# Kernel tuning notes

Hardware: AMD Instinct MI355X
Metric: run time of the kernel (lower is better)

The kernel has to match this reference:

```python
import jax, jax.numpy as jnp
import numpy as np

B = 4
S = 1024          # per-sequence length (equal for all sequences)
HQ = 32           # query heads
HK = 8            # kv heads (GQA)
D = 128           # head dim


def setup_inputs() -> dict:
    key = jax.random.key(0)
    k1, k2, k3 = jax.random.split(key, 3)
    total = B * S
    q = jax.random.normal(k1, (total, HQ, D), dtype=jnp.float32)
    k = jax.random.normal(k2, (total, HK, D), dtype=jnp.float32)
    v = jax.random.normal(k3, (total, HK, D), dtype=jnp.float32)
    cu = (jnp.arange(B + 1, dtype=jnp.int32) * S)
    return {
        "q": q, "k": k, "v": v,
        "cu_seqlens_q": cu, "cu_seqlens_k": cu,
        "max_seqlen_q": S, "max_seqlen_k": S,
    }


def reference(q, k, v, cu_seqlens_q, cu_seqlens_k, max_seqlen_q, max_seqlen_k):
    # Varlen causal GQA attention (prefill path of Attention.forward).
    # All sequences have equal length S = max_seqlen_q, so the packed varlen
    # layout is exactly a reshape to (B, S, H, D) -- same math as the
    # per-sequence Python loop in attention_varlen_func.
    total, Hq, Dh = q.shape
    Hk = k.shape[1]
    g = Hq // Hk                      # GQA group size
    Sq = int(max_seqlen_q)
    Bn = total // Sq
    scale = 1.0 / (Dh ** 0.5)

    qb = q.reshape(Bn, Sq, Hk, g, Dh)  # (B,S,Hk,g,D)
    kb = k.reshape(Bn, Sq, Hk, Dh)     # (B,S,Hk,D)
    vb = v.reshape(Bn, Sq, Hk, Dh)

    scores = jnp.einsum('bqhgd,bkhd->bhgqk', qb, kb) * scale  # (B,Hk,g,S,S)
    causal_mask = jnp.triu(jnp.ones((Sq, Sq), dtype=bool), k=1)
    scores = jnp.where(causal_mask, -jnp.inf, scores)
    attn = jax.nn.softmax(scores, axis=-1)
    out = jnp.einsum('bhgqk,bkhd->bqhgd', attn, vb)           # (B,S,Hk,g,D)
    return out.reshape(total, Hq, Dh)
```

## Files before the change

### kernel.cpp

```cpp
#include <hip/hip_runtime.h>
#include <hip/hip_bf16.h>
#include <stdint.h>


typedef __bf16 v8bf __attribute__((ext_vector_type(8)));
typedef __bf16 v4bf __attribute__((ext_vector_type(4)));
typedef float  v16f __attribute__((ext_vector_type(16)));

#define NB  4
#define NS  1024
#define NHQ 32
#define NHK 8
#define ND  128
#define BQ  128
#define BK  64
#define VOFF (8u << 20)

#define KOFF(r) (16*((r)>>3) + ((((r)>>2)&1)*4) + ((r)&3))

__global__ __launch_bounds__(256)
void prep(const float* __restrict__ kg, const float* __restrict__ vg,
          char* __restrict__ ws)
{
  const int tid = threadIdx.x;
  const int blk = blockIdx.x;
  if (blk < 4096) {
    int gid = blk * 256 + tid;
    int i  = gid & 31;
    int s  = (gid >> 5) & (NS - 1);
    int hk = (gid >> 15) & 7;
    int b  = gid >> 18;
    float4 f = *(const float4*)(kg + ((size_t)((b * NS + s) * NHK + hk)) * ND + 4 * i);
    v4bf kb;
    kb[0]=(__bf16)f.x; kb[1]=(__bf16)f.y; kb[2]=(__bf16)f.z; kb[3]=(__bf16)f.w;
    int t  = s >> 6;
    int c  = (s >> 5) & 1;
    int kk = s & 31;
    int mu = (kk & 3) + 4 * ((kk >> 3) & 1)
           + 8 * (2 * ((kk >> 4) & 1) + ((kk >> 2) & 1));
    int fidx  = c * 8 + (i >> 2);
    int halfb = (i >> 1) & 1;
    int byte  = fidx * 1024 + halfb * 512 + mu * 16 + ((4 * i) & 7) * 2;
    size_t tb = (size_t)((b * 8 + hk) * 16 + t) << 14;
    *(v4bf*)(ws + tb + byte) = kb;
  } else {
    int vid = (blk - 4096) * 256 + tid;
    int d  = vid & 127;
    int g  = (vid >> 7) & 7;
    int t  = (vid >> 10) & 15;
    int hk = (vid >> 14) & 7;
    int b  = vid >> 17;
    const float* vp = vg + ((size_t)((b * NS + t * 64 + g * 8) * NHK + hk)) * ND + d;
    v8bf w;
    #pragma unroll
    for (int e = 0; e < 8; ++e) w[e] = (__bf16)vp[(size_t)e * (NHK * ND)];
    int byte = (d * 8 + (g ^ ((d >> 1) & 7))) * 16;
    size_t tb = (size_t)((b * 8 + hk) * 16 + t) << 14;
    *(v8bf*)(ws + VOFF + tb + byte) = w;
  }
}

__global__ __launch_bounds__(256, 2)
void fattn(const float* __restrict__ qg, const char* __restrict__ kvg,
           float* __restrict__ og)
{
  __shared__ __align__(16) char  Vt[2][16384];
  __shared__ __align__(16) float alq[4 * 32];

  const int tid  = threadIdx.x;
  const int lane = tid & 63;
  const int wave = tid >> 6;
  const int half = lane >> 5;
  const int l31  = lane & 31;

  const int bx = blockIdx.x;
  const int hk = bx & 7;
  const int t6 = bx >> 3;
  const int b  = t6 >> 4;
  const int m6 = t6 & 15;
  const int p  = m6 >> 2;
  const int h  = hk * 4 + (m6 & 3);

  const float scale = 0.12751879523604785f;
  const int kvtile = (b * 8 + hk) * 16;

  auto dmaV = [&](int t_, char* dst) {
    const char* src = kvg + VOFF + ((size_t)(kvtile + t_) << 14);
    #pragma unroll
    for (int i = 0; i < 4; ++i) {
      int c = wave * 4 + i;
      __builtin_amdgcn_global_load_lds(
        (const __attribute__((address_space(1))) void*)(src + c * 1024 + lane * 16),
        (__attribute__((address_space(3))) void*)(dst + c * 1024),
        16, 0, 0);
    }
  };

  dmaV(0, Vt[0]);
  int cur = 0;

  for (int ph = 0; ph < 2; ++ph) {
    const int qt = ph ? (7 - p) : p;
    const int wv = ph ? (3 - wave) : wave;
    const int q0 = qt * BQ;
    const int wqb = q0 + wv * 32;
    const int qglob = wqb + l31;
    const int ntiles = 2 * (qt + 1);

    v8bf qf[8];
    {
      const float* qp = qg + ((size_t)((b * NS + qglob) * NHQ + h)) * ND + half * 8;
      #pragma unroll
      for (int dM = 0; dM < 8; ++dM) {
        float4 f0 = *(const float4*)(qp + dM * 16);
        float4 f1 = *(const float4*)(qp + dM * 16 + 4);
        v8bf t;
        t[0]=(__bf16)(f0.x*scale); t[1]=(__bf16)(f0.y*scale);
        t[2]=(__bf16)(f0.z*scale); t[3]=(__bf16)(f0.w*scale);
        t[4]=(__bf16)(f1.x*scale); t[5]=(__bf16)(f1.y*scale);
        t[6]=(__bf16)(f1.z*scale); t[7]=(__bf16)(f1.w*scale);
        qf[dM] = t;
      }
    }

    v16f accO[4];
    #pragma unroll
    for (int dt = 0; dt < 4; ++dt)
      #pragma unroll
      for (int e = 0; e < 16; ++e) accO[dt][e] = 0.f;
    float m_run = -INFINITY, l_run = 0.f;

    for (int t = 0; t < ntiles; ++t) {
      const int k0 = t * BK;

      asm volatile("s_waitcnt vmcnt(0)" ::: "memory");
      __syncthreads();

      if (t + 1 < ntiles)      dmaV(t + 1, Vt[cur ^ 1]);
      else if (ph == 0)        dmaV(0, Vt[cur ^ 1]);

      if (k0 <= wqb + 31) {
        const v8bf* kf = (const v8bf*)(kvg + ((size_t)(kvtile + t) << 14) + lane * 16);
        v8bf ka0[8], ka1[8];
        #pragma unroll
        for (int f = 0; f < 8; ++f) ka0[f] = kf[(size_t)f * 64];
        #pragma unroll
        for (int f = 0; f < 8; ++f) ka1[f] = kf[(size_t)(f + 8) * 64];

        v16f s0, s1;
        #pragma unroll
        for (int e = 0; e < 16; ++e) { s0[e] = 0.f; s1[e] = 0.f; }
        __builtin_amdgcn_s_setprio(1);
        #pragma unroll
        for (int dM = 0; dM < 8; ++dM)
          s0 = __builtin_amdgcn_mfma_f32_32x32x16_bf16(ka0[dM], qf[dM], s0, 0, 0, 0);
        #pragma unroll
        for (int dM = 0; dM < 8; ++dM)
          s1 = __builtin_amdgcn_mfma_f32_32x32x16_bf16(ka1[dM], qf[dM], s1, 0, 0, 0);
        __builtin_amdgcn_s_setprio(0);
        if (k0 + BK > wqb) {
          #pragma unroll
          for (int r = 0; r < 16; ++r) {
            int key = k0 + KOFF(r) + half * 8;
            if (key > qglob)      s0[r] = -INFINITY;
            if (key + 32 > qglob) s1[r] = -INFINITY;
          }
        }
        float m0 = s0[0];
        #pragma unroll
        for (int r = 1; r < 16; ++r) m0 = fmaxf(m0, s0[r]);
        #pragma unroll
        for (int r = 0; r < 16; ++r) m0 = fmaxf(m0, s1[r]);
        m0 = fmaxf(m0, __shfl_xor(m0, 32));
        float mn = fmaxf(m_run, m0);
        float rs = 0.f;
        #pragma unroll
        for (int r = 0; r < 16; ++r) { float pp = exp2f(s0[r] - mn); s0[r] = pp; rs += pp; }
        #pragma unroll
        for (int r = 0; r < 16; ++r) { float pp = exp2f(s1[r] - mn); s1[r] = pp; rs += pp; }
        rs += __shfl_xor(rs, 32);
        if (__any(m0 > m_run)) {
          float al = exp2f(m_run - mn);
          if (half == 0) alq[wave * 32 + l31] = al;
          float4 alf[4];
          #pragma unroll
          for (int c = 0; c < 4; ++c)
            alf[c] = *(const float4*)(&alq[wave * 32 + 8 * c + 4 * half]);
          #pragma unroll
          for (int dt = 0; dt < 4; ++dt)
            #pragma unroll
            for (int r = 0; r < 16; ++r)
              accO[dt][r] *= ((const float*)&alf[r >> 2])[r & 3];
          l_run = l_run * al + rs;
        } else {
          l_run += rs;
        }
        m_run = mn;
        const char* vtr = Vt[cur];
        __builtin_amdgcn_s_setprio(1);
        #pragma unroll
        for (int C = 0; C < 2; ++C) {
          #pragma unroll
          for (int cp = 0; cp < 2; ++cp) {
            v8bf pf;
            #pragma unroll
            for (int e = 0; e < 8; ++e)
              pf[e] = (__bf16)(C == 0 ? s0[cp * 8 + e] : s1[cp * 8 + e]);
            int g = (C * 2 + cp) * 2 + half;
            #pragma unroll
            for (int dt = 0; dt < 4; ++dt) {
              int d = dt * 32 + l31;
              v8bf vb = *(const v8bf*)(vtr + (d * 8 + (g ^ ((l31 >> 1) & 7))) * 16);
              accO[dt] = __builtin_amdgcn_mfma_f32_32x32x16_bf16(pf, vb, accO[dt], 0, 0, 0);
            }
          }
        }
        __builtin_amdgcn_s_setprio(0);
      }
      cur ^= 1;
    }

    if (half == 0) alq[wave * 32 + l31] = 1.f / l_run;
    float4 invf[4];
    #pragma unroll
    for (int c = 0; c < 4; ++c)
      invf[c] = *(const float4*)(&alq[wave * 32 + 8 * c + 4 * half]);
    #pragma unroll
    for (int dt = 0; dt < 4; ++dt) {
      #pragma unroll
      for (int r = 0; r < 16; ++r) {
        int qrow = (r & 3) + 8 * (r >> 2) + 4 * half;
        float* op = og + ((size_t)((b * NS + wqb + qrow) * NHQ + h)) * ND;
        op[dt * 32 + l31] = accO[dt][r] * ((const float*)&invf[r >> 2])[r & 3];
      }
    }
  }
}

extern "C" void kernel_launch(void* const* d_in, const int* in_sizes, int n_in,
                              void* d_out, int out_size, void* d_ws, size_t ws_size,
                              hipStream_t stream) {
  const float* q = (const float*)d_in[0];
  const float* k = (const float*)d_in[1];
  const float* v = (const float*)d_in[2];
  float* out = (float*)d_out;
  char* ws = (char*)d_ws;
  prep<<<dim3(4096 + 2048), 256, 0, stream>>>(k, v, ws);
  fattn<<<dim3(NB * NHQ * 4), 256, 0, stream>>>(q, ws, out);
}
```

Before: 200.3 us.

## Split KV range across two wave groups with LDS-staged K/V and merge

Doubles the block to 512 threads so two groups of four waves each process alternate 32-key tiles, then merges their softmax states and partial outputs through shared memory. K and V for a tile are interleaved in one 16KB workspace block and DMA'd together into LDS, replacing the per-wave global K loads. The exp is switched to a raw v_exp_f32, and the max and sum reductions become trees. This aims for more waves in flight and better latency hiding, but it adds an epilogue merge with three extra barriers and smaller per-wave tiles.

New measurement: 297.0 us. +48.3%, slower.

```diff
diff --git a/kernel.cpp b/kernel.cpp
--- a/kernel.cpp
+++ b/kernel.cpp
@@ -13,10 +13,13 @@
 #define NHK 8
 #define ND  128
 #define BQ  128
-#define BK  64
-#define VOFF (8u << 20)
+#define BK  32
 
 #define KOFF(r) (16*((r)>>3) + ((((r)>>2)&1)*4) + ((r)&3))
+
+__device__ __forceinline__ float fexp2(float x) {
+  float r; asm("v_exp_f32 %0, %1" : "=v"(r) : "v"(x)); return r;
+}
 
 __global__ __launch_bounds__(256)
 void prep(const float* __restrict__ kg, const float* __restrict__ vg,
@@ -33,45 +36,48 @@
     float4 f = *(const float4*)(kg + ((size_t)((b * NS + s) * NHK + hk)) * ND + 4 * i);
     v4bf kb;
     kb[0]=(__bf16)f.x; kb[1]=(__bf16)f.y; kb[2]=(__bf16)f.z; kb[3]=(__bf16)f.w;
-    int t  = s >> 6;
-    int c  = (s >> 5) & 1;
+    int t  = s >> 5;
     int kk = s & 31;
     int mu = (kk & 3) + 4 * ((kk >> 3) & 1)
            + 8 * (2 * ((kk >> 4) & 1) + ((kk >> 2) & 1));
-    int fidx  = c * 8 + (i >> 2);
+    int dM    = i >> 2;
     int halfb = (i >> 1) & 1;
-    int byte  = fidx * 1024 + halfb * 512 + mu * 16 + ((4 * i) & 7) * 2;
-    size_t tb = (size_t)((b * 8 + hk) * 16 + t) << 14;
+    int byte  = dM * 1024 + halfb * 512 + mu * 16 + ((4 * i) & 7) * 2;
+    size_t tb = (size_t)((b * 8 + hk) * 32 + t) << 14;
     *(v4bf*)(ws + tb + byte) = kb;
   } else {
     int vid = (blk - 4096) * 256 + tid;
     int d  = vid & 127;
-    int g  = (vid >> 7) & 7;
-    int t  = (vid >> 10) & 15;
+    int g  = (vid >> 7) & 3;
+    int t  = (vid >> 9) & 31;
     int hk = (vid >> 14) & 7;
     int b  = vid >> 17;
-    const float* vp = vg + ((size_t)((b * NS + t * 64 + g * 8) * NHK + hk)) * ND + d;
+    const float* vp = vg + ((size_t)((b * NS + t * 32 + g * 8) * NHK + hk)) * ND + d;
     v8bf w;
     #pragma unroll
     for (int e = 0; e < 8; ++e) w[e] = (__bf16)vp[(size_t)e * (NHK * ND)];
-    int byte = (d * 8 + (g ^ ((d >> 1) & 7))) * 16;
-    size_t tb = (size_t)((b * 8 + hk) * 16 + t) << 14;
-    *(v8bf*)(ws + VOFF + tb + byte) = w;
+    int byte = (d >> 1) * 128 + ((g ^ ((d >> 1) & 3)) * 32) + (d & 1) * 16;
+    size_t tb = (size_t)((b * 8 + hk) * 32 + t) << 14;
+    *(v8bf*)(ws + tb + 8192 + byte) = w;
   }
 }
 
-__global__ __launch_bounds__(256, 2)
+__global__ __launch_bounds__(512, 4)
 void fattn(const float* __restrict__ qg, const char* __restrict__ kvg,
            float* __restrict__ og)
 {
-  __shared__ __align__(16) char  Vt[2][16384];
-  __shared__ __align__(16) float alq[4 * 32];
+  __shared__ __align__(16) char  KV[2][32768];
+  __shared__ __align__(16) float alq[8 * 32];
+  __shared__ __align__(16) float mex[2 * 4 * 32];
+  __shared__ __align__(16) float lex[2 * 4 * 32];
 
   const int tid  = threadIdx.x;
   const int lane = tid & 63;
   const int wave = tid >> 6;
   const int half = lane >> 5;
   const int l31  = lane & 31;
+  const int rs4  = wave & 3;
+  const int kh   = wave >> 2;
 
   const int bx = blockIdx.x;
   const int hk = bx & 7;
@@ -82,10 +88,10 @@
   const int h  = hk * 4 + (m6 & 3);
 
   const float scale = 0.12751879523604785f;
-  const int kvtile = (b * 8 + hk) * 16;
-
-  auto dmaV = [&](int t_, char* dst) {
-    const char* src = kvg + VOFF + ((size_t)(kvtile + t_) << 14);
+  const int kvtile = (b * 8 + hk) * 32;
+
+  auto dma = [&](int s_, char* dst) {
+    const char* src = kvg + ((size_t)(kvtile + 2 * s_) << 14);
     #pragma unroll
     for (int i = 0; i < 4; ++i) {
       int c = wave * 4 + i;
@@ -96,16 +102,16 @@
     }
   };
 
-  dmaV(0, Vt[0]);
-  int cur = 0;
-
   for (int ph = 0; ph < 2; ++ph) {
     const int qt = ph ? (7 - p) : p;
-    const int wv = ph ? (3 - wave) : wave;
+    const int rv = ph ? (3 - rs4) : rs4;
     const int q0 = qt * BQ;
-    const int wqb = q0 + wv * 32;
+    const int wqb = q0 + rv * 32;
     const int qglob = wqb + l31;
-    const int ntiles = 2 * (qt + 1);
+    const int nsteps = 2 * (qt + 1);
+
+    dma(0, KV[0]);
+    int cur = 0;
 
     v8bf qf[8];
     {
@@ -130,57 +136,48 @@
       for (int e = 0; e < 16; ++e) accO[dt][e] = 0.f;
     float m_run = -INFINITY, l_run = 0.f;
 
-    for (int t = 0; t < ntiles; ++t) {
-      const int k0 = t * BK;
-
+    for (int s = 0; s < nsteps; ++s) {
       asm volatile("s_waitcnt vmcnt(0)" ::: "memory");
       __syncthreads();
-
-      if (t + 1 < ntiles)      dmaV(t + 1, Vt[cur ^ 1]);
-      else if (ph == 0)        dmaV(0, Vt[cur ^ 1]);
-
-      if (k0 <= wqb + 31) {
-        const v8bf* kf = (const v8bf*)(kvg + ((size_t)(kvtile + t) << 14) + lane * 16);
-        v8bf ka0[8], ka1[8];
-        #pragma unroll
-        for (int f = 0; f < 8; ++f) ka0[f] = kf[(size_t)f * 64];
-        #pragma unroll
-        for (int f = 0; f < 8; ++f) ka1[f] = kf[(size_t)(f + 8) * 64];
-
-        v16f s0, s1;
-        #pragma unroll
-        for (int e = 0; e < 16; ++e) { s0[e] = 0.f; s1[e] = 0.f; }
+      if (s + 1 < nsteps) dma(s + 1, KV[cur ^ 1]);
+
+      const int k0w = (2 * s + kh) * 32;
+      if (k0w <= wqb + 31) {
+        const char* kb = KV[cur] + kh * 16384;
+        v16f s0;
+        #pragma unroll
+        for (int e = 0; e < 16; ++e) s0[e] = 0.f;
         __builtin_amdgcn_s_setprio(1);
         #pragma unroll
-        for (int dM = 0; dM < 8; ++dM)
-          s0 = __builtin_amdgcn_mfma_f32_32x32x16_bf16(ka0[dM], qf[dM], s0, 0, 0, 0);
-        #pragma unroll
-        for (int dM = 0; dM < 8; ++dM)
-          s1 = __builtin_amdgcn_mfma_f32_32x32x16_bf16(ka1[dM], qf[dM], s1, 0, 0, 0);
+        for (int dM = 0; dM < 8; ++dM) {
+          v8bf ka = *(const v8bf*)(kb + dM * 1024 + lane * 16);
+          s0 = __builtin_amdgcn_mfma_f32_32x32x16_bf16(ka, qf[dM], s0, 0, 0, 0);
+        }
         __builtin_amdgcn_s_setprio(0);
-        if (k0 + BK > wqb) {
-          #pragma unroll
-          for (int r = 0; r < 16; ++r) {
-            int key = k0 + KOFF(r) + half * 8;
-            if (key > qglob)      s0[r] = -INFINITY;
-            if (key + 32 > qglob) s1[r] = -INFINITY;
-          }
-        }
-        float m0 = s0[0];
-        #pragma unroll
-        for (int r = 1; r < 16; ++r) m0 = fmaxf(m0, s0[r]);
-        #pragma unroll
-        for (int r = 0; r < 16; ++r) m0 = fmaxf(m0, s1[r]);
+        if (k0w + BK > wqb) {
+          #pragma unroll
+          for (int r = 0; r < 16; ++r)
+            if (k0w + KOFF(r) + half * 8 > qglob) s0[r] = -INFINITY;
+        }
+        float t8[8];
+        #pragma unroll
+        for (int i = 0; i < 8; ++i) t8[i] = fmaxf(s0[i], s0[i + 8]);
+        #pragma unroll
+        for (int i = 0; i < 4; ++i) t8[i] = fmaxf(t8[i], t8[i + 4]);
+        float m0 = fmaxf(fmaxf(t8[0], t8[2]), fmaxf(t8[1], t8[3]));
         m0 = fmaxf(m0, __shfl_xor(m0, 32));
         float mn = fmaxf(m_run, m0);
-        float rs = 0.f;
-        #pragma unroll
-        for (int r = 0; r < 16; ++r) { float pp = exp2f(s0[r] - mn); s0[r] = pp; rs += pp; }
-        #pragma unroll
-        for (int r = 0; r < 16; ++r) { float pp = exp2f(s1[r] - mn); s1[r] = pp; rs += pp; }
+        #pragma unroll
+        for (int r = 0; r < 16; ++r) s0[r] = fexp2(s0[r] - mn);
+        float u8[8];
+        #pragma unroll
+        for (int i = 0; i < 8; ++i) u8[i] = s0[i] + s0[i + 8];
+        #pragma unroll
+        for (int i = 0; i < 4; ++i) u8[i] = u8[i] + u8[i + 4];
+        float rs = (u8[0] + u8[2]) + (u8[1] + u8[3]);
         rs += __shfl_xor(rs, 32);
         if (__any(m0 > m_run)) {
-          float al = exp2f(m_run - mn);
+          float al = fexp2(m_run - mn);
           if (half == 0) alq[wave * 32 + l31] = al;
           float4 alf[4];
           #pragma unroll
@@ -196,23 +193,19 @@
           l_run += rs;
         }
         m_run = mn;
-        const char* vtr = Vt[cur];
         __builtin_amdgcn_s_setprio(1);
         #pragma unroll
-        for (int C = 0; C < 2; ++C) {
-          #pragma unroll
-          for (int cp = 0; cp < 2; ++cp) {
-            v8bf pf;
-            #pragma unroll
-            for (int e = 0; e < 8; ++e)
-              pf[e] = (__bf16)(C == 0 ? s0[cp * 8 + e] : s1[cp * 8 + e]);
-            int g = (C * 2 + cp) * 2 + half;
-            #pragma unroll
-            for (int dt = 0; dt < 4; ++dt) {
-              int d = dt * 32 + l31;
-              v8bf vb = *(const v8bf*)(vtr + (d * 8 + (g ^ ((l31 >> 1) & 7))) * 16);
-              accO[dt] = __builtin_amdgcn_mfma_f32_32x32x16_bf16(pf, vb, accO[dt], 0, 0, 0);
-            }
+        for (int cp = 0; cp < 2; ++cp) {
+          v8bf pf;
+          #pragma unroll
+          for (int e = 0; e < 8; ++e) pf[e] = (__bf16)s0[cp * 8 + e];
+          int g = cp * 2 + half;
+          #pragma unroll
+          for (int dt = 0; dt < 4; ++dt) {
+            int dh = dt * 16 + (l31 >> 1);
+            v8bf vb = *(const v8bf*)(kb + 8192 + dh * 128
+                        + ((g ^ (dh & 3)) * 32) + (l31 & 1) * 16);
+            accO[dt] = __builtin_amdgcn_mfma_f32_32x32x16_bf16(pf, vb, accO[dt], 0, 0, 0);
           }
         }
         __builtin_amdgcn_s_setprio(0);
@@ -220,18 +213,70 @@
       cur ^= 1;
     }
 
-    if (half == 0) alq[wave * 32 + l31] = 1.f / l_run;
-    float4 invf[4];
-    #pragma unroll
-    for (int c = 0; c < 4; ++c)
-      invf[c] = *(const float4*)(&alq[wave * 32 + 8 * c + 4 * half]);
-    #pragma unroll
-    for (int dt = 0; dt < 4; ++dt) {
-      #pragma unroll
-      for (int r = 0; r < 16; ++r) {
-        int qrow = (r & 3) + 8 * (r >> 2) + 4 * half;
-        float* op = og + ((size_t)((b * NS + wqb + qrow) * NHQ + h)) * ND;
-        op[dt * 32 + l31] = accO[dt][r] * ((const float*)&invf[r >> 2])[r & 3];
+    if (half == 0) mex[(kh * 4 + rs4) * 32 + l31] = m_run;
+    __syncthreads();
+    float m_oth = mex[((kh ^ 1) * 4 + rs4) * 32 + l31];
+    float M = fmaxf(m_run, m_oth);
+    float a = fexp2(m_run - M);
+    float lw = l_run * a;
+    if (half == 0) { alq[wave * 32 + l31] = a; lex[(kh * 4 + rs4) * 32 + l31] = lw; }
+    {
+      float4 af[4];
+      #pragma unroll
+      for (int c = 0; c < 4; ++c)
+        af[c] = *(const float4*)(&alq[wave * 32 + 8 * c + 4 * half]);
+      #pragma unroll
+      for (int dt = 0; dt < 4; ++dt)
+        #pragma unroll
+        for (int r = 0; r < 16; ++r)
+          accO[dt][r] *= ((const float*)&af[r >> 2])[r & 3];
+    }
+    float* mscr = (float*)&KV[0][0];
+    if (kh == 1) {
+      #pragma unroll
+      for (int dt = 0; dt < 4; ++dt) {
+        int col = dt * 32 + l31;
+        #pragma unroll
+        for (int q = 0; q < 4; ++q) {
+          int qi = 2 * q + half;
+          float4 w = make_float4(accO[dt][4*q], accO[dt][4*q+1],
+                                 accO[dt][4*q+2], accO[dt][4*q+3]);
+          *(float4*)(mscr + rs4 * 4096 + col * 32 + ((qi ^ (col & 7)) << 2)) = w;
+        }
+      }
+    }
+    __syncthreads();
+    float l_fin = 1.f;
+    if (kh == 0) {
+      l_fin = lw + lex[(4 + rs4) * 32 + l31];
+      #pragma unroll
+      for (int dt = 0; dt < 4; ++dt) {
+        int col = dt * 32 + l31;
+        #pragma unroll
+        for (int q = 0; q < 4; ++q) {
+          int qi = 2 * q + half;
+          float4 r4 = *(const float4*)(mscr + rs4 * 4096 + col * 32 + ((qi ^ (col & 7)) << 2));
+          accO[dt][4*q]   += r4.x; accO[dt][4*q+1] += r4.y;
+          accO[dt][4*q+2] += r4.z; accO[dt][4*q+3] += r4.w;
+        }
+      }
+    }
+    __syncthreads();
+
+    if (kh == 0) {
+      if (half == 0) alq[wave * 32 + l31] = 1.f / l_fin;
+      float4 invf[4];
+      #pragma unroll
+      for (int c = 0; c < 4; ++c)
+        invf[c] = *(const float4*)(&alq[wave * 32 + 8 * c + 4 * half]);
+      #pragma unroll
+      for (int dt = 0; dt < 4; ++dt) {
+        #pragma unroll
+        for (int r = 0; r < 16; ++r) {
+          int qrow = (r & 3) + 8 * (r >> 2) + 4 * half;
+          float* op = og + ((size_t)((b * NS + wqb + qrow) * NHQ + h)) * ND;
+          op[dt * 32 + l31] = accO[dt][r] * ((const float*)&invf[r >> 2])[r & 3];
+        }
       }
     }
   }
@@ -246,5 +291,5 @@
   float* out = (float*)d_out;
   char* ws = (char*)d_ws;
   prep<<<dim3(4096 + 2048), 256, 0, stream>>>(k, v, ws);
-  fattn<<<dim3(NB * NHQ * 4), 256, 0, stream>>>(q, ws, out);
-}
+  fattn<<<dim3(NB * NHQ * 4), 512, 0, stream>>>(q, ws, out);
+}
```
